# Performance work log

Hardware: AMD Instinct MI355X
Metric: run time of the kernel (lower is better)

The kernel has to match this reference:

```python
import jax, jax.numpy as jnp
import numpy as np

B, T, D = 128, 512, 300  # batch, timeframe, embedding/context dim

def setup_inputs() -> dict:
    key = jax.random.key(0)
    ks = jax.random.split(key, 5)
    s = 1.0 / np.sqrt(600.0)
    return {
        "x": jax.random.normal(ks[0], (B, T, D), dtype=jnp.float32),
        "W1": jax.random.uniform(ks[1], (D, 2 * D), dtype=jnp.float32, minval=-s, maxval=s),
        "b1": jax.random.uniform(ks[2], (D,), dtype=jnp.float32, minval=-s, maxval=s),
        "W2": jax.random.uniform(ks[3], (D, D), dtype=jnp.float32, minval=-s, maxval=s),
        "b2": jax.random.uniform(ks[4], (D,), dtype=jnp.float32, minval=-s, maxval=s),
    }

def reference(x, W1, b1, W2, b2):
    # Elman cell per step: lin1 = [x_t, h] @ W1^T + b1; h <- lin1 (pre-activation!);
    # out_t = sigmoid(lin1) @ W2^T + b2
    batch = x.shape[0]
    h0 = jnp.zeros((batch, x.shape[2]), dtype=x.dtype)
    # split W1 into input and hidden parts to avoid per-step concat
    Wx = W1[:, : x.shape[2]]   # (D, D)
    Wh = W1[:, x.shape[2]:]    # (D, D)
    # precompute input projections for all timesteps: (B,T,D)
    xproj = jnp.einsum('btd,cd->btc', x, Wx) + b1

    def step(h, xp_t):
        lin1 = xp_t + h @ Wh.T          # (B, D)
        out_t = jax.nn.sigmoid(lin1) @ W2.T + b2
        return lin1, out_t

    hidden, outs = jax.lax.scan(step, h0, jnp.swapaxes(xproj, 0, 1))
    outputs = jnp.swapaxes(outs, 0, 1)  # (B, T, D)
    return outputs, hidden
```

## Files before the change

### kernel.cpp

```cpp
#include <hip/hip_runtime.h>


typedef _Float16 half2_t __attribute__((ext_vector_type(2)));
typedef _Float16 half4_t __attribute__((ext_vector_type(4)));
typedef _Float16 half8_t __attribute__((ext_vector_type(8)));
typedef float f32x4 __attribute__((ext_vector_type(4)));

#define NCOL 300
#define NPADT 304
#define B_   128
#define T_   512
#define NROWS ((size_t)B_ * T_)

template <int AIN_F16, int COUT_F16>
__global__ __launch_bounds__(256, 2) void gemm_kernel(
    const void* __restrict__ Ain, const float* __restrict__ W, int ldw,
    int koff, const float* __restrict__ bias, void* __restrict__ Cout) {
  __shared__ __align__(16) _Float16 Alds[128 * 40];
  __shared__ __align__(16) _Float16 Blds[NPADT * 40];

  const int tid = threadIdx.x;
  const size_t m0 = (size_t)blockIdx.x * 128;
  const int lane = tid & 63, wv = tid >> 6;
  const int lr = lane & 15, quad = lane >> 4;

  f32x4 acc[2][19];
#pragma unroll
  for (int mt = 0; mt < 2; ++mt)
#pragma unroll
    for (int nt = 0; nt < 19; ++nt) acc[mt][nt] = (f32x4){0.f, 0.f, 0.f, 0.f};

  const int srow = tid >> 1;
  const int shalf = tid & 1;

  for (int k0 = 0; k0 < 320; k0 += 32) {
    __syncthreads();
    {
      const int gk = k0 + shalf * 16;
      _Float16 v[16];
      if (AIN_F16) {
        const _Float16* ap = (const _Float16*)Ain + (m0 + srow) * NPADT + gk;
        if (gk < NPADT) {
          half8_t u0 = *(const half8_t*)ap;
          half8_t u1 = *(const half8_t*)(ap + 8);
#pragma unroll
          for (int i = 0; i < 8; ++i) { v[i] = u0[i]; v[8 + i] = u1[i]; }
        } else {
#pragma unroll
          for (int i = 0; i < 16; ++i) v[i] = (_Float16)0.f;
        }
      } else {
        const float* ap = (const float*)Ain + (m0 + srow) * NCOL + gk;
        if (gk + 15 < NCOL) {
#pragma unroll
          for (int q = 0; q < 4; ++q) {
            float4 f = ((const float4*)ap)[q];
            v[4 * q + 0] = (_Float16)f.x; v[4 * q + 1] = (_Float16)f.y;
            v[4 * q + 2] = (_Float16)f.z; v[4 * q + 3] = (_Float16)f.w;
          }
        } else {
#pragma unroll
          for (int i = 0; i < 16; ++i)
            v[i] = (gk + i < NCOL) ? (_Float16)ap[i] : (_Float16)0.f;
        }
      }
      half8_t* dst = (half8_t*)(Alds + srow * 40 + shalf * 16);
      dst[0] = (half8_t){v[0], v[1], v[2], v[3], v[4], v[5], v[6], v[7]};
      dst[1] = (half8_t){v[8], v[9], v[10], v[11], v[12], v[13], v[14], v[15]};
    }
#pragma unroll
    for (int p = 0; p < 3; ++p) {
      const int n = p * 128 + srow;
      if (n < NPADT) {
        const int gk = k0 + shalf * 16;
        _Float16 v[16];
        const float* wp = W + (size_t)n * ldw + koff + gk;
        if (n < NCOL && gk + 15 < NCOL) {
#pragma unroll
          for (int q = 0; q < 4; ++q) {
            float4 f = ((const float4*)wp)[q];
            v[4 * q + 0] = (_Float16)f.x; v[4 * q + 1] = (_Float16)f.y;
            v[4 * q + 2] = (_Float16)f.z; v[4 * q + 3] = (_Float16)f.w;
          }
        } else {
#pragma unroll
          for (int i = 0; i < 16; ++i)
            v[i] = (n < NCOL && gk + i < NCOL) ? (_Float16)wp[i]
                                               : (_Float16)0.f;
        }
        half8_t* dst = (half8_t*)(Blds + n * 40 + shalf * 16);
        dst[0] = (half8_t){v[0], v[1], v[2], v[3], v[4], v[5], v[6], v[7]};
        dst[1] = (half8_t){v[8], v[9], v[10], v[11], v[12], v[13], v[14], v[15]};
      }
    }
    __syncthreads();
    half8_t a0 = *(const half8_t*)(Alds + (wv * 32 + lr) * 40 + quad * 8);
    half8_t a1 = *(const half8_t*)(Alds + (wv * 32 + 16 + lr) * 40 + quad * 8);
#pragma unroll
    for (int nt = 0; nt < 19; ++nt) {
      half8_t b = *(const half8_t*)(Blds + (nt * 16 + lr) * 40 + quad * 8);
      acc[0][nt] = __builtin_amdgcn_mfma_f32_16x16x32_f16(a0, b, acc[0][nt], 0, 0, 0);
      acc[1][nt] = __builtin_amdgcn_mfma_f32_16x16x32_f16(a1, b, acc[1][nt], 0, 0, 0);
    }
  }

  const size_t rowbase = m0 + (size_t)wv * 32;
#pragma unroll
  for (int nt = 0; nt < 19; ++nt) {
    const int n = nt * 16 + lr;
    const float bv = (n < NCOL) ? bias[n] : 0.f;
#pragma unroll
    for (int mt = 0; mt < 2; ++mt) {
#pragma unroll
      for (int reg = 0; reg < 4; ++reg) {
        const size_t row = rowbase + mt * 16 + quad * 4 + reg;
        const float val = acc[mt][nt][reg] + bv;
        if (COUT_F16) {
          ((_Float16*)Cout)[row * NPADT + n] = (_Float16)val;
        } else if (n < NCOL) {
          ((float*)Cout)[row * NCOL + n] = val;
        }
      }
    }
  }
}

#define LCH 16
#define WRM 48
#define HSTR 328

__global__ __launch_bounds__(256, 1) void scan_mfma_kernel(
    const float* __restrict__ W1, const _Float16* __restrict__ XP,
    _Float16* __restrict__ P, float* __restrict__ hidden) {
  __shared__ __align__(16) _Float16 hb[2][16 * HSTR];
  const int tid = threadIdx.x;
  const int lane = tid & 63, wv = tid >> 6;
  const int lr = lane & 15, quad = lane >> 4;
  const int bg = blockIdx.x & 7;
  const int ch = blockIdx.x >> 3;
  const int t0 = ch * LCH;
  const int ts = (t0 > WRM) ? (t0 - WRM) : 0;
  const int tend = t0 + LCH;

  half8_t af[5][10];
#pragma unroll
  for (int i = 0; i < 5; ++i) {
    const int tt = wv * 5 + i;
    const int col = tt * 16 + lr;
#pragma unroll
    for (int kk = 0; kk < 10; ++kk) {
      const int kb = kk * 32 + quad * 8;
      half8_t v;
#pragma unroll
      for (int j = 0; j < 8; ++j) v[j] = (_Float16)0.f;
      if (tt < 19 && col < NCOL) {
        const float* wp = W1 + (size_t)col * 600 + 300 + kb;
        if (kb + 7 < NCOL) {
          float4 f0 = ((const float4*)wp)[0];
          float4 f1 = ((const float4*)wp)[1];
          v[0] = (_Float16)f0.x; v[1] = (_Float16)f0.y;
          v[2] = (_Float16)f0.z; v[3] = (_Float16)f0.w;
          v[4] = (_Float16)f1.x; v[5] = (_Float16)f1.y;
          v[6] = (_Float16)f1.z; v[7] = (_Float16)f1.w;
        } else {
#pragma unroll
          for (int j = 0; j < 8; ++j)
            if (kb + j < NCOL) v[j] = (_Float16)wp[j];
        }
      }
      af[i][kk] = v;
    }
  }

  {
    _Float16* hz = &hb[0][0];
    half8_t z;
#pragma unroll
    for (int j = 0; j < 8; ++j) z[j] = (_Float16)0.f;
    for (int i = tid * 8; i < 2 * 16 * HSTR; i += 2048) *(half8_t*)(hz + i) = z;
  }
  __syncthreads();

  const int batch = bg * 16 + lr;
  const _Float16* xpb = XP + (size_t)batch * T_ * NPADT;
  _Float16* pb = P + (size_t)batch * T_ * NPADT;

  int colb[5];
  bool tv[5];
#pragma unroll
  for (int i = 0; i < 5; ++i) {
    const int tt = wv * 5 + i;
    tv[i] = (tt < 19);
    colb[i] = (tt < 19) ? (tt * 16 + quad * 4) : 0;
  }

  half4_t xq[5];
#pragma unroll
  for (int i = 0; i < 5; ++i) {
    half4_t z;
    z[0] = z[1] = z[2] = z[3] = (_Float16)0.f;
    xq[i] = tv[i] ? *(const half4_t*)(xpb + (size_t)ts * NPADT + colb[i]) : z;
  }

  int p = 0;
  for (int t = ts; t < tend; ++t) {
    const _Float16* hrow = hb[p] + lr * HSTR;
    half8_t bf[10];
#pragma unroll
    for (int kk = 0; kk < 10; ++kk)
      bf[kk] = *(const half8_t*)(hrow + kk * 32 + quad * 8);

    half4_t xc[5];
#pragma unroll
    for (int i = 0; i < 5; ++i) xc[i] = xq[i];
    if (t + 1 < tend) {
#pragma unroll
      for (int i = 0; i < 5; ++i)
        if (tv[i])
          xq[i] = *(const half4_t*)(xpb + (size_t)(t + 1) * NPADT + colb[i]);
    }

    f32x4 acc[5];
#pragma unroll
    for (int i = 0; i < 5; ++i) acc[i] = (f32x4){0.f, 0.f, 0.f, 0.f};
#pragma unroll
    for (int kk = 0; kk < 10; ++kk)
#pragma unroll
      for (int i = 0; i < 5; ++i)
        acc[i] =
            __builtin_amdgcn_mfma_f32_16x16x32_f16(af[i][kk], bf[kk], acc[i], 0, 0, 0);

    _Float16* hw = hb[p ^ 1] + lr * HSTR;
    const bool emit = (t >= t0);
#pragma unroll
    for (int i = 0; i < 5; ++i) {
      const float l0 = acc[i][0] + (float)xc[i][0];
      const float l1 = acc[i][1] + (float)xc[i][1];
      const float l2 = acc[i][2] + (float)xc[i][2];
      const float l3 = acc[i][3] + (float)xc[i][3];
      if (tv[i]) {
        half4_t hv;
        hv[0] = (_Float16)l0; hv[1] = (_Float16)l1;
        hv[2] = (_Float16)l2; hv[3] = (_Float16)l3;
        *(half4_t*)(hw + colb[i]) = hv;
        if (emit) {
          half4_t sv;
          sv[0] = (_Float16)(1.f / (1.f + __expf(-l0)));
          sv[1] = (_Float16)(1.f / (1.f + __expf(-l1)));
          sv[2] = (_Float16)(1.f / (1.f + __expf(-l2)));
          sv[3] = (_Float16)(1.f / (1.f + __expf(-l3)));
          *(half4_t*)(pb + (size_t)t * NPADT + colb[i]) = sv;
          if (t == T_ - 1) {
            float* hd = hidden + (size_t)batch * NCOL + colb[i];
            if (colb[i] + 3 < NCOL) {
              *(float4*)hd = (float4){l0, l1, l2, l3};
            } else {
              if (colb[i] + 0 < NCOL) hd[0] = l0;
              if (colb[i] + 1 < NCOL) hd[1] = l1;
              if (colb[i] + 2 < NCOL) hd[2] = l2;
              if (colb[i] + 3 < NCOL) hd[3] = l3;
            }
          }
        }
      }
    }
    __syncthreads();
    p ^= 1;
  }
}

extern "C" void kernel_launch(void* const* d_in, const int* in_sizes, int n_in,
                              void* d_out, int out_size, void* d_ws,
                              size_t ws_size, hipStream_t stream) {
  const float* x  = (const float*)d_in[0];
  const float* W1 = (const float*)d_in[1];
  const float* b1 = (const float*)d_in[2];
  const float* W2 = (const float*)d_in[3];
  const float* b2 = (const float*)d_in[4];
  float* out = (float*)d_out;
  float* hidden = out + NROWS * NCOL;

  _Float16* XP = (_Float16*)d_ws;
  _Float16* P  = XP + NROWS * NPADT;

  gemm_kernel<0, 1><<<512, 256, 0, stream>>>(x, W1, 600, 0, b1, XP);
  scan_mfma_kernel<<<256, 256, 0, stream>>>(W1, XP, P, hidden);
  gemm_kernel<1, 0><<<512, 256, 0, stream>>>(P, W2, 300, 0, b2, out);
}
```

Before: 345.1 us.

## Rewrite projection GEMMs to load operands directly into registers without LDS

```diff
diff --git a/kernel.cpp b/kernel.cpp
--- a/kernel.cpp
+++ b/kernel.cpp
@@ -12,114 +12,127 @@
 #define T_   512
 #define NROWS ((size_t)B_ * T_)
 
-template <int AIN_F16, int COUT_F16>
-__global__ __launch_bounds__(256, 2) void gemm_kernel(
-    const void* __restrict__ Ain, const float* __restrict__ W, int ldw,
-    int koff, const float* __restrict__ bias, void* __restrict__ Cout) {
-  __shared__ __align__(16) _Float16 Alds[128 * 40];
-  __shared__ __align__(16) _Float16 Blds[NPADT * 40];
-
+__device__ __forceinline__ half8_t zero8() {
+  half8_t v;
+#pragma unroll
+  for (int j = 0; j < 8; ++j) v[j] = (_Float16)0.f;
+  return v;
+}
+
+__device__ __forceinline__ half8_t cvt8(const float* __restrict__ p) {
+  float4 f0 = *(const float4*)p;
+  float4 f1 = *(const float4*)(p + 4);
+  half8_t v;
+  v[0] = (_Float16)f0.x; v[1] = (_Float16)f0.y;
+  v[2] = (_Float16)f0.z; v[3] = (_Float16)f0.w;
+  v[4] = (_Float16)f1.x; v[5] = (_Float16)f1.y;
+  v[6] = (_Float16)f1.z; v[7] = (_Float16)f1.w;
+  return v;
+}
+
+template <int BF32, int CF16>
+__global__ __launch_bounds__(256, 2) void gemm2_kernel(
+    const float* __restrict__ W, int ldw, const void* __restrict__ Bd,
+    const float* __restrict__ bias, void* __restrict__ Cd) {
   const int tid = threadIdx.x;
-  const size_t m0 = (size_t)blockIdx.x * 128;
   const int lane = tid & 63, wv = tid >> 6;
   const int lr = lane & 15, quad = lane >> 4;
-
-  f32x4 acc[2][19];
-#pragma unroll
-  for (int mt = 0; mt < 2; ++mt)
-#pragma unroll
-    for (int nt = 0; nt < 19; ++nt) acc[mt][nt] = (f32x4){0.f, 0.f, 0.f, 0.f};
-
-  const int srow = tid >> 1;
-  const int shalf = tid & 1;
-
-  for (int k0 = 0; k0 < 320; k0 += 32) {
-    __syncthreads();
-    {
-      const int gk = k0 + shalf * 16;
-      _Float16 v[16];
-      if (AIN_F16) {
-        const _Float16* ap = (const _Float16*)Ain + (m0 + srow) * NPADT + gk;
-        if (gk < NPADT) {
-          half8_t u0 = *(const half8_t*)ap;
-          half8_t u1 = *(const half8_t*)(ap + 8);
-#pragma unroll
-          for (int i = 0; i < 8; ++i) { v[i] = u0[i]; v[8 + i] = u1[i]; }
+  const int kq = quad * 8;
+  const size_t rowbase = (size_t)blockIdx.x * 128 + (size_t)wv * 32;
+
+  f32x4 acc[19][2];
+#pragma unroll
+  for (int ct = 0; ct < 19; ++ct)
+#pragma unroll
+    for (int rt = 0; rt < 2; ++rt) acc[ct][rt] = (f32x4){0.f, 0.f, 0.f, 0.f};
+
+  const size_t row0 = rowbase + lr;
+  const size_t row1 = rowbase + 16 + lr;
+
+#pragma unroll
+  for (int k0 = 0; k0 < 10; ++k0) {
+    const int kb = k0 * 32 + kq;
+    const bool tail = (k0 == 9);
+
+    half8_t bf[2];
+#pragma unroll
+    for (int rt = 0; rt < 2; ++rt) {
+      const size_t row = rt ? row1 : row0;
+      if (BF32) {
+        const float* bp = (const float*)Bd + row * NCOL;
+        if (!tail) {
+          bf[rt] = cvt8(bp + kb);
         } else {
-#pragma unroll
-          for (int i = 0; i < 16; ++i) v[i] = (_Float16)0.f;
+          half8_t v = zero8();
+#pragma unroll
+          for (int j = 0; j < 8; ++j)
+            if (kb + j < NCOL) v[j] = (_Float16)bp[kb + j];
+          bf[rt] = v;
         }
       } else {
-        const float* ap = (const float*)Ain + (m0 + srow) * NCOL + gk;
-        if (gk + 15 < NCOL) {
-#pragma unroll
-          for (int q = 0; q < 4; ++q) {
-            float4 f = ((const float4*)ap)[q];
-            v[4 * q + 0] = (_Float16)f.x; v[4 * q + 1] = (_Float16)f.y;
-            v[4 * q + 2] = (_Float16)f.z; v[4 * q + 3] = (_Float16)f.w;
+        const _Float16* bp = (const _Float16*)Bd + row * NPADT;
+        if (!tail) {
+          bf[rt] = *(const half8_t*)(bp + kb);
+        } else {
+          bf[rt] = (kb + 7 < NPADT) ? *(const half8_t*)(bp + kb) : zero8();
+        }
+      }
+    }
+
+#pragma unroll
+    for (int h = 0; h < 2; ++h) {
+      const int c0 = h * 10;
+      const int cn = h ? 9 : 10;
+      half8_t af[10];
+#pragma unroll
+      for (int i = 0; i < cn; ++i) {
+        const int ct = c0 + i;
+        const int wr = ct * 16 + lr;
+        const bool ok = (wr < NCOL);
+        if (!tail) {
+          af[i] = ok ? cvt8(W + (size_t)wr * ldw + kb) : zero8();
+        } else {
+          half8_t v = zero8();
+          if (ok) {
+            const float* wp = W + (size_t)wr * ldw;
+#pragma unroll
+            for (int j = 0; j < 8; ++j)
+              if (kb + j < NCOL) v[j] = (_Float16)wp[kb + j];
           }
-        } else {
-#pragma unroll
-          for (int i = 0; i < 16; ++i)
-            v[i] = (gk + i < NCOL) ? (_Float16)ap[i] : (_Float16)0.f;
-        }
-      }
-      half8_t* dst = (half8_t*)(Alds + srow * 40 + shalf * 16);
-      dst[0] = (half8_t){v[0], v[1], v[2], v[3], v[4], v[5], v[6], v[7]};
-      dst[1] = (half8_t){v[8], v[9], v[10], v[11], v[12], v[13], v[14], v[15]};
-    }
-#pragma unroll
-    for (int p = 0; p < 3; ++p) {
-      const int n = p * 128 + srow;
-      if (n < NPADT) {
-        const int gk = k0 + shalf * 16;
-        _Float16 v[16];
-        const float* wp = W + (size_t)n * ldw + koff + gk;
-        if (n < NCOL && gk + 15 < NCOL) {
-#pragma unroll
-          for (int q = 0; q < 4; ++q) {
-            float4 f = ((const float4*)wp)[q];
-            v[4 * q + 0] = (_Float16)f.x; v[4 * q + 1] = (_Float16)f.y;
-            v[4 * q + 2] = (_Float16)f.z; v[4 * q + 3] = (_Float16)f.w;
-          }
-        } else {
-#pragma unroll
-          for (int i = 0; i < 16; ++i)
-            v[i] = (n < NCOL && gk + i < NCOL) ? (_Float16)wp[i]
-                                               : (_Float16)0.f;
-        }
-        half8_t* dst = (half8_t*)(Blds + n * 40 + shalf * 16);
-        dst[0] = (half8_t){v[0], v[1], v[2], v[3], v[4], v[5], v[6], v[7]};
-        dst[1] = (half8_t){v[8], v[9], v[10], v[11], v[12], v[13], v[14], v[15]};
-      }
-    }
-    __syncthreads();
-    half8_t a0 = *(const half8_t*)(Alds + (wv * 32 + lr) * 40 + quad * 8);
-    half8_t a1 = *(const half8_t*)(Alds + (wv * 32 + 16 + lr) * 40 + quad * 8);
-#pragma unroll
-    for (int nt = 0; nt < 19; ++nt) {
-      half8_t b = *(const half8_t*)(Blds + (nt * 16 + lr) * 40 + quad * 8);
-      acc[0][nt] = __builtin_amdgcn_mfma_f32_16x16x32_f16(a0, b, acc[0][nt], 0, 0, 0);
-      acc[1][nt] = __builtin_amdgcn_mfma_f32_16x16x32_f16(a1, b, acc[1][nt], 0, 0, 0);
-    }
-  }
-
-  const size_t rowbase = m0 + (size_t)wv * 32;
-#pragma unroll
-  for (int nt = 0; nt < 19; ++nt) {
-    const int n = nt * 16 + lr;
-    const float bv = (n < NCOL) ? bias[n] : 0.f;
-#pragma unroll
-    for (int mt = 0; mt < 2; ++mt) {
-#pragma unroll
-      for (int reg = 0; reg < 4; ++reg) {
-        const size_t row = rowbase + mt * 16 + quad * 4 + reg;
-        const float val = acc[mt][nt][reg] + bv;
-        if (COUT_F16) {
-          ((_Float16*)Cout)[row * NPADT + n] = (_Float16)val;
-        } else if (n < NCOL) {
-          ((float*)Cout)[row * NCOL + n] = val;
-        }
+          af[i] = v;
+        }
+      }
+#pragma unroll
+      for (int i = 0; i < cn; ++i) {
+#pragma unroll
+        for (int rt = 0; rt < 2; ++rt)
+          acc[c0 + i][rt] = __builtin_amdgcn_mfma_f32_16x16x32_f16(
+              af[i], bf[rt], acc[c0 + i][rt], 0, 0, 0);
+      }
+    }
+  }
+
+#pragma unroll
+  for (int ct = 0; ct < 19; ++ct) {
+    const int col0 = ct * 16 + quad * 4;
+    float4 bv;
+    if (col0 <= 296) bv = *(const float4*)(bias + col0);
+    else bv = (float4){0.f, 0.f, 0.f, 0.f};
+#pragma unroll
+    for (int rt = 0; rt < 2; ++rt) {
+      const size_t row = rt ? row1 : row0;
+      const float v0 = acc[ct][rt][0] + bv.x;
+      const float v1 = acc[ct][rt][1] + bv.y;
+      const float v2 = acc[ct][rt][2] + bv.z;
+      const float v3 = acc[ct][rt][3] + bv.w;
+      if (CF16) {
+        half4_t hv;
+        hv[0] = (_Float16)v0; hv[1] = (_Float16)v1;
+        hv[2] = (_Float16)v2; hv[3] = (_Float16)v3;
+        *(half4_t*)((_Float16*)Cd + row * NPADT + col0) = hv;
+      } else if (col0 <= 296) {
+        *(float4*)((float*)Cd + row * NCOL + col0) =
+            (float4){v0, v1, v2, v3};
       }
     }
   }
@@ -283,7 +296,7 @@
   _Float16* XP = (_Float16*)d_ws;
   _Float16* P  = XP + NROWS * NPADT;
 
-  gemm_kernel<0, 1><<<512, 256, 0, stream>>>(x, W1, 600, 0, b1, XP);
+  gemm2_kernel<1, 1><<<512, 256, 0, stream>>>(W1, 600, x, b1, XP);
   scan_mfma_kernel<<<256, 256, 0, stream>>>(W1, XP, P, hidden);
-  gemm_kernel<1, 0><<<512, 256, 0, stream>>>(P, W2, 300, 0, b2, out);
-}
+  gemm2_kernel<0, 0><<<512, 256, 0, stream>>>(W2, 300, P, b2, out);
+}
```

After: 500.3 us. +45.0%, slower.

## Pre-pack fp16 weights, double-buffer GEMM with direct global-to-LDS loads, swizzle scan LDS

Applied to the files above, without the earlier changes.

```diff
diff --git a/kernel.cpp b/kernel.cpp
--- a/kernel.cpp
+++ b/kernel.cpp
@@ -1,7 +1,6 @@
 #include <hip/hip_runtime.h>
 
 
-typedef _Float16 half2_t __attribute__((ext_vector_type(2)));
 typedef _Float16 half4_t __attribute__((ext_vector_type(4)));
 typedef _Float16 half8_t __attribute__((ext_vector_type(8)));
 typedef float f32x4 __attribute__((ext_vector_type(4)));
@@ -12,17 +11,56 @@
 #define T_   512
 #define NROWS ((size_t)B_ * T_)
 
+#define WFH  12160
+#define WFCH 1520
+
+__device__ __forceinline__ half8_t zero8() {
+  half8_t v;
+#pragma unroll
+  for (int j = 0; j < 8; ++j) v[j] = (_Float16)0.f;
+  return v;
+}
+
+__device__ __forceinline__ void gl_lds16(const _Float16* g, _Float16* l) {
+  __builtin_amdgcn_global_load_lds(
+      (const __attribute__((address_space(1))) void*)g,
+      (__attribute__((address_space(3))) void*)l, 16, 0, 0);
+}
+
+__global__ void prep_w_kernel(const float* __restrict__ W, int ldw,
+                              _Float16* __restrict__ Wf) {
+  const int k0 = blockIdx.x;
+  const int row = threadIdx.x;
+  if (row >= NPADT) return;
+  half8_t v8[5];
+#pragma unroll
+  for (int q = 0; q < 5; ++q) v8[q] = zero8();
+  if (row < NCOL) {
+    const int kb = k0 * 32;
+    const float* wp = W + (size_t)row * ldw;
+#pragma unroll
+    for (int j = 0; j < 32; ++j) {
+      const int k = kb + j;
+      if (k < NCOL) v8[j >> 3][j & 7] = (_Float16)wp[k];
+    }
+  }
+  half8_t* dst = (half8_t*)(Wf + (size_t)k0 * WFH + row * 40);
+#pragma unroll
+  for (int q = 0; q < 5; ++q) dst[q] = v8[q];
+}
+
 template <int AIN_F16, int COUT_F16>
-__global__ __launch_bounds__(256, 2) void gemm_kernel(
-    const void* __restrict__ Ain, const float* __restrict__ W, int ldw,
-    int koff, const float* __restrict__ bias, void* __restrict__ Cout) {
-  __shared__ __align__(16) _Float16 Alds[128 * 40];
-  __shared__ __align__(16) _Float16 Blds[NPADT * 40];
+__global__ __launch_bounds__(256, 2) void gemm3_kernel(
+    const void* __restrict__ Ain, const _Float16* __restrict__ Wf,
+    const float* __restrict__ bias, void* __restrict__ Cout) {
+  __shared__ __align__(16) _Float16 Alds[2][128 * 40];
+  __shared__ __align__(16) _Float16 Blds[2][WFH];
 
   const int tid = threadIdx.x;
-  const size_t m0 = (size_t)blockIdx.x * 128;
   const int lane = tid & 63, wv = tid >> 6;
   const int lr = lane & 15, quad = lane >> 4;
+  const size_t m0 = (size_t)blockIdx.x * 128;
+  const int srow = tid >> 1, shalf = tid & 1;
 
   f32x4 acc[2][19];
 #pragma unroll
@@ -30,78 +68,79 @@
 #pragma unroll
     for (int nt = 0; nt < 19; ++nt) acc[mt][nt] = (f32x4){0.f, 0.f, 0.f, 0.f};
 
-  const int srow = tid >> 1;
-  const int shalf = tid & 1;
-
-  for (int k0 = 0; k0 < 320; k0 += 32) {
-    __syncthreads();
-    {
-      const int gk = k0 + shalf * 16;
-      _Float16 v[16];
-      if (AIN_F16) {
-        const _Float16* ap = (const _Float16*)Ain + (m0 + srow) * NPADT + gk;
-        if (gk < NPADT) {
-          half8_t u0 = *(const half8_t*)ap;
-          half8_t u1 = *(const half8_t*)(ap + 8);
-#pragma unroll
-          for (int i = 0; i < 8; ++i) { v[i] = u0[i]; v[8 + i] = u1[i]; }
-        } else {
-#pragma unroll
-          for (int i = 0; i < 16; ++i) v[i] = (_Float16)0.f;
+  auto stage_b = [&](int buf, int kk0) {
+    const _Float16* src = Wf + (size_t)kk0 * WFH;
+    _Float16* dstb = &Blds[buf][(tid & 192) * 8];
+#pragma unroll
+    for (int r = 0; r < 6; ++r) {
+      const int id = r * 256 + tid;
+      if (id < WFCH) gl_lds16(src + (size_t)id * 8, dstb + r * 2048);
+    }
+  };
+
+  float fa[16];
+  half8_t haf[2];
+  auto load_a = [&](int kk0) {
+    const int gk = kk0 * 32 + shalf * 16;
+    if (AIN_F16) {
+      const _Float16* ap = (const _Float16*)Ain + (m0 + srow) * NPADT + gk;
+      if (gk + 15 < NPADT) {
+        haf[0] = ((const half8_t*)ap)[0];
+        haf[1] = ((const half8_t*)ap)[1];
+      } else {
+        haf[0] = zero8(); haf[1] = zero8();
+      }
+    } else {
+      const float* ap = (const float*)Ain + (m0 + srow) * NCOL + gk;
+      if (gk + 15 < NCOL) {
+#pragma unroll
+        for (int q = 0; q < 4; ++q) {
+          float4 f = ((const float4*)ap)[q];
+          fa[4 * q + 0] = f.x; fa[4 * q + 1] = f.y;
+          fa[4 * q + 2] = f.z; fa[4 * q + 3] = f.w;
         }
       } else {
-        const float* ap = (const float*)Ain + (m0 + srow) * NCOL + gk;
-        if (gk + 15 < NCOL) {
-#pragma unroll
-          for (int q = 0; q < 4; ++q) {
-            float4 f = ((const float4*)ap)[q];
-            v[4 * q + 0] = (_Float16)f.x; v[4 * q + 1] = (_Float16)f.y;
-            v[4 * q + 2] = (_Float16)f.z; v[4 * q + 3] = (_Float16)f.w;
-          }
-        } else {
-#pragma unroll
-          for (int i = 0; i < 16; ++i)
-            v[i] = (gk + i < NCOL) ? (_Float16)ap[i] : (_Float16)0.f;
-        }
-      }
-      half8_t* dst = (half8_t*)(Alds + srow * 40 + shalf * 16);
-      dst[0] = (half8_t){v[0], v[1], v[2], v[3], v[4], v[5], v[6], v[7]};
-      dst[1] = (half8_t){v[8], v[9], v[10], v[11], v[12], v[13], v[14], v[15]};
-    }
-#pragma unroll
-    for (int p = 0; p < 3; ++p) {
-      const int n = p * 128 + srow;
-      if (n < NPADT) {
-        const int gk = k0 + shalf * 16;
-        _Float16 v[16];
-        const float* wp = W + (size_t)n * ldw + koff + gk;
-        if (n < NCOL && gk + 15 < NCOL) {
-#pragma unroll
-          for (int q = 0; q < 4; ++q) {
-            float4 f = ((const float4*)wp)[q];
-            v[4 * q + 0] = (_Float16)f.x; v[4 * q + 1] = (_Float16)f.y;
-            v[4 * q + 2] = (_Float16)f.z; v[4 * q + 3] = (_Float16)f.w;
-          }
-        } else {
-#pragma unroll
-          for (int i = 0; i < 16; ++i)
-            v[i] = (n < NCOL && gk + i < NCOL) ? (_Float16)wp[i]
-                                               : (_Float16)0.f;
-        }
-        half8_t* dst = (half8_t*)(Blds + n * 40 + shalf * 16);
-        dst[0] = (half8_t){v[0], v[1], v[2], v[3], v[4], v[5], v[6], v[7]};
-        dst[1] = (half8_t){v[8], v[9], v[10], v[11], v[12], v[13], v[14], v[15]};
-      }
-    }
-    __syncthreads();
-    half8_t a0 = *(const half8_t*)(Alds + (wv * 32 + lr) * 40 + quad * 8);
-    half8_t a1 = *(const half8_t*)(Alds + (wv * 32 + 16 + lr) * 40 + quad * 8);
+#pragma unroll
+        for (int j = 0; j < 16; ++j)
+          fa[j] = (gk + j < NCOL) ? ap[j] : 0.f;
+      }
+    }
+  };
+  auto write_a = [&](int buf) {
+    half8_t u0, u1;
+    if (AIN_F16) {
+      u0 = haf[0]; u1 = haf[1];
+    } else {
+#pragma unroll
+      for (int j = 0; j < 8; ++j) { u0[j] = (_Float16)fa[j]; u1[j] = (_Float16)fa[8 + j]; }
+    }
+    half8_t* d = (half8_t*)(Alds[buf] + srow * 40 + shalf * 16);
+    d[0] = u0; d[1] = u1;
+  };
+
+  stage_b(0, 0);
+  load_a(0);
+  write_a(0);
+  __syncthreads();
+
+  int cur = 0;
+#pragma unroll
+  for (int k0 = 0; k0 < 10; ++k0) {
+    if (k0 < 9) {
+      stage_b(cur ^ 1, k0 + 1);
+      load_a(k0 + 1);
+    }
+    half8_t a0 = *(const half8_t*)(Alds[cur] + (wv * 32 + lr) * 40 + quad * 8);
+    half8_t a1 = *(const half8_t*)(Alds[cur] + (wv * 32 + 16 + lr) * 40 + quad * 8);
 #pragma unroll
     for (int nt = 0; nt < 19; ++nt) {
-      half8_t b = *(const half8_t*)(Blds + (nt * 16 + lr) * 40 + quad * 8);
+      half8_t b = *(const half8_t*)(Blds[cur] + (nt * 16 + lr) * 40 + quad * 8);
       acc[0][nt] = __builtin_amdgcn_mfma_f32_16x16x32_f16(a0, b, acc[0][nt], 0, 0, 0);
       acc[1][nt] = __builtin_amdgcn_mfma_f32_16x16x32_f16(a1, b, acc[1][nt], 0, 0, 0);
     }
+    if (k0 < 9) write_a(cur ^ 1);
+    __syncthreads();
+    cur ^= 1;
   }
 
   const size_t rowbase = m0 + (size_t)wv * 32;
@@ -127,7 +166,7 @@
 
 #define LCH 16
 #define WRM 48
-#define HSTR 328
+#define HSTR 384
 
 __global__ __launch_bounds__(256, 1) void scan_mfma_kernel(
     const float* __restrict__ W1, const _Float16* __restrict__ XP,
@@ -136,6 +175,7 @@
   const int tid = threadIdx.x;
   const int lane = tid & 63, wv = tid >> 6;
   const int lr = lane & 15, quad = lane >> 4;
+  const int swz = (lr & 7) << 3;
   const int bg = blockIdx.x & 7;
   const int ch = blockIdx.x >> 3;
   const int t0 = ch * LCH;
@@ -150,9 +190,7 @@
 #pragma unroll
     for (int kk = 0; kk < 10; ++kk) {
       const int kb = kk * 32 + quad * 8;
-      half8_t v;
-#pragma unroll
-      for (int j = 0; j < 8; ++j) v[j] = (_Float16)0.f;
+      half8_t v = zero8();
       if (tt < 19 && col < NCOL) {
         const float* wp = W1 + (size_t)col * 600 + 300 + kb;
         if (kb + 7 < NCOL) {
@@ -174,9 +212,7 @@
 
   {
     _Float16* hz = &hb[0][0];
-    half8_t z;
-#pragma unroll
-    for (int j = 0; j < 8; ++j) z[j] = (_Float16)0.f;
+    half8_t z = zero8();
     for (int i = tid * 8; i < 2 * 16 * HSTR; i += 2048) *(half8_t*)(hz + i) = z;
   }
   __syncthreads();
@@ -194,12 +230,15 @@
     colb[i] = (tt < 19) ? (tt * 16 + quad * 4) : 0;
   }
 
-  half4_t xq[5];
+  half4_t xq0[5], xq1[5];
 #pragma unroll
   for (int i = 0; i < 5; ++i) {
     half4_t z;
     z[0] = z[1] = z[2] = z[3] = (_Float16)0.f;
-    xq[i] = tv[i] ? *(const half4_t*)(xpb + (size_t)ts * NPADT + colb[i]) : z;
+    xq0[i] = tv[i] ? *(const half4_t*)(xpb + (size_t)ts * NPADT + colb[i]) : z;
+    xq1[i] = (tv[i] && ts + 1 < tend)
+                 ? *(const half4_t*)(xpb + (size_t)(ts + 1) * NPADT + colb[i])
+                 : z;
   }
 
   int p = 0;
@@ -208,16 +247,16 @@
     half8_t bf[10];
 #pragma unroll
     for (int kk = 0; kk < 10; ++kk)
-      bf[kk] = *(const half8_t*)(hrow + kk * 32 + quad * 8);
+      bf[kk] = *(const half8_t*)(hrow + ((kk * 32 + quad * 8) ^ swz));
 
     half4_t xc[5];
 #pragma unroll
-    for (int i = 0; i < 5; ++i) xc[i] = xq[i];
-    if (t + 1 < tend) {
+    for (int i = 0; i < 5; ++i) { xc[i] = xq0[i]; xq0[i] = xq1[i]; }
+    if (t + 2 < tend) {
 #pragma unroll
       for (int i = 0; i < 5; ++i)
         if (tv[i])
-          xq[i] = *(const half4_t*)(xpb + (size_t)(t + 1) * NPADT + colb[i]);
+          xq1[i] = *(const half4_t*)(xpb + (size_t)(t + 2) * NPADT + colb[i]);
     }
 
     f32x4 acc[5];
@@ -242,7 +281,7 @@
         half4_t hv;
         hv[0] = (_Float16)l0; hv[1] = (_Float16)l1;
         hv[2] = (_Float16)l2; hv[3] = (_Float16)l3;
-        *(half4_t*)(hw + colb[i]) = hv;
+        *(half4_t*)(hw + (colb[i] ^ swz)) = hv;
         if (emit) {
           half4_t sv;
           sv[0] = (_Float16)(1.f / (1.f + __expf(-l0)));
@@ -283,7 +322,12 @@
   _Float16* XP = (_Float16*)d_ws;
   _Float16* P  = XP + NROWS * NPADT;
 
-  gemm_kernel<0, 1><<<512, 256, 0, stream>>>(x, W1, 600, 0, b1, XP);
+  _Float16* Wf1 = P;
+  _Float16* Wf2 = XP;
+
+  prep_w_kernel<<<10, 320, 0, stream>>>(W1, 600, Wf1);
+  gemm3_kernel<0, 1><<<512, 256, 0, stream>>>(x, Wf1, b1, XP);
   scan_mfma_kernel<<<256, 256, 0, stream>>>(W1, XP, P, hidden);
-  gemm_kernel<1, 0><<<512, 256, 0, stream>>>(P, W2, 300, 0, b2, out);
-}
+  prep_w_kernel<<<10, 320, 0, stream>>>(W2, 300, Wf2);
+  gemm3_kernel<1, 0><<<512, 256, 0, stream>>>(P, Wf2, b2, out);
+}
```

Result: no change. 340.2 us (-1.4%).
